# Kernel optimization log

Measured on AMD Instinct MI355X. Metric: run time of the kernel, lower is better.

Reference implementation:

```python
import jax, jax.numpy as jnp
import numpy as np

B, S, E = 4, 2048, 1024


def setup_inputs() -> dict:
    key = jax.random.key(0)
    ks = jax.random.split(key, 7)
    s = 1.0 / np.sqrt(E)  # torch Linear default init scale (uniform bound)
    inp = {
        "input": jax.random.normal(ks[0], (B, S, E), dtype=jnp.float32),
        "masked": 1,
        "W_q": jax.random.uniform(ks[1], (E, E), jnp.float32, -s, s),
        "b_q": jax.random.uniform(ks[2], (E,), jnp.float32, -s, s),
        "W_k": jax.random.uniform(ks[3], (E, E), jnp.float32, -s, s),
        "b_k": jax.random.uniform(ks[4], (E,), jnp.float32, -s, s),
        "W_v": jax.random.uniform(ks[5], (E, E), jnp.float32, -s, s),
        "b_v": jax.random.uniform(ks[6], (E,), jnp.float32, -s, s),
    }
    return inp


def reference(input, masked, W_q, b_q, W_k, b_k, W_v, b_v):
    # torch.nn.Linear: y = x @ W.T + b
    q = jnp.einsum("bse,fe->bsf", input, W_q) + b_q
    k = jnp.einsum("bse,fe->bsf", input, W_k) + b_k
    v = jnp.einsum("bse,fe->bsf", input, W_v) + b_v
    d = q.shape[-1]
    scores = jnp.einsum("bqd,bkd->bqk", q, k) / jnp.sqrt(jnp.float32(d))
    if masked:
        Sq = scores.shape[1]
        causal = jnp.tril(jnp.ones((Sq, Sq), dtype=bool))  # [S,S], broadcast over batch
        scores = jnp.where(causal, scores, -jnp.inf)
    attn = jax.nn.softmax(scores, axis=-1)
    return jnp.einsum("bqk,bkd->bqd", attn, v)
```

## Files before the change

### kernel.cpp

```cpp
#include <hip/hip_runtime.h>

typedef _Float16 f16;
typedef f16 f16x8 __attribute__((ext_vector_type(8)));
typedef f16 f16x4v __attribute__((ext_vector_type(4)));
typedef f16 f16x2v __attribute__((ext_vector_type(2)));
typedef float f32x4 __attribute__((ext_vector_type(4)));

__device__ __forceinline__ void async_ld16(const void* g, void* l) {
    __builtin_amdgcn_global_load_lds(
        (const __attribute__((address_space(1))) unsigned int*)g,
        (__attribute__((address_space(3))) unsigned int*)l, 16, 0, 0);
}

#define VMC(n) asm volatile("s_waitcnt vmcnt(" #n ")" ::: "memory")
#define BAR __builtin_amdgcn_s_barrier()


#define STG(b, op, kh, P, P1, tOff) do {                                        \
    char* d_ = (char*)smem + (b) * 65536 + (op) * 32768 + (kh) * 16384 + stgBase; \
    async_ld16((P)  + (tOff) * 64 + (kh) * 32, d_);                             \
    async_ld16((P1) + (tOff) * 64 + (kh) * 32, d_ + 8192);                      \
} while (0)
#define RD_A(b, kk) do {                                                        \
    const char* s_ = (const char*)smem + (b) * 65536 + (kk) * 16384 + aOff;     \
    _Pragma("unroll") for (int m_ = 0; m_ < 8; ++m_)                            \
        af[m_] = *(const f16x8*)(s_ + m_ * 1024);                               \
} while (0)
#define RD_B2(b, kk, n0_) do {                                                  \
    const char* s_ = (const char*)smem + (b) * 65536 + 32768 + (kk) * 16384 + bOff; \
    bf[(n0_)]     = *(const f16x8*)(s_ + ((n0_)) * 1024);                       \
    bf[(n0_) + 1] = *(const f16x8*)(s_ + ((n0_) + 1) * 1024);                   \
} while (0)
#define FENCE_MM(n0_) do {                                                      \
    __builtin_amdgcn_s_barrier();                                               \
    asm volatile("s_waitcnt lgkmcnt(0)" ::: "memory");                          \
    __builtin_amdgcn_sched_barrier(0);                                          \
    __builtin_amdgcn_s_setprio(1);                                              \
    _Pragma("unroll") for (int m_ = 0; m_ < 8; ++m_) {                          \
        acc[m_][(n0_)]     = __builtin_amdgcn_mfma_f32_16x16x32_f16(af[m_], bf[(n0_)],     acc[m_][(n0_)],     0, 0, 0); \
        acc[m_][(n0_) + 1] = __builtin_amdgcn_mfma_f32_16x16x32_f16(af[m_], bf[(n0_) + 1], acc[m_][(n0_) + 1], 0, 0, 0); \
    }                                                                           \
    __builtin_amdgcn_s_setprio(0);                                              \
} while (0)

__global__ __launch_bounds__(512, 2) void scores256(
    const f16* __restrict__ Q, const f16* __restrict__ K,
    f16* __restrict__ P, const int* __restrict__ maskedp)
{
    const int masked = *maskedp;
    const int bx = blockIdx.x, by = blockIdx.y, bz = blockIdx.z;
    if (masked && bx > by) return;
    const int mBase = by * 256, nBase = bx * 256;

    __shared__ __align__(16) f16 smem[65536];
    const int tid = threadIdx.x;
    const int wave = tid >> 6, lane = tid & 63;
    const int wrow = wave >> 2, wcol = wave & 3;
    const int quad = lane >> 4, l16 = lane & 15;
    const int rowLane = tid >> 2;
    const int cOff = ((tid & 3) ^ ((tid >> 3) & 3)) * 8;
    const int stgBase = wave * 1024;
    const int swz  = (quad ^ ((l16 >> 1) & 3)) * 16;
    const int aOff = (wrow * 128 + l16) * 64 + swz;
    const int bOff = (wcol * 64 + l16) * 64 + swz;
    f32x4 acc[8][4];
#pragma unroll
    for (int m = 0; m < 8; ++m)
#pragma unroll
        for (int n = 0; n < 4; ++n) acc[m][n] = (f32x4){0.f, 0.f, 0.f, 0.f};
    f16x8 af[8], bf[4];

    const f16* Ab  = Q + (long)bz * (2048L * 1024);
    const f16* Btb = K + (long)bz * (2048L * 1024);
    const f16* pA  = Ab  + (long)(mBase + rowLane) * 1024 + cOff;
    const f16* pA1 = pA + 128 * 1024;
    const f16* pB  = Btb + (long)(nBase + rowLane) * 1024 + cOff;
    const f16* pB1 = pB + 128 * 1024;

    STG(0, 0, 0, pA, pA1, 0); STG(0, 1, 0, pB, pB1, 0);
    STG(0, 0, 1, pA, pA1, 0); STG(0, 1, 1, pB, pB1, 0);
    STG(1, 0, 0, pA, pA1, 1); STG(1, 1, 0, pB, pB1, 1);
    VMC(4);
    BAR;

#pragma unroll 1
    for (int i = 0; i < 7; ++i) {
        RD_A(0, 0); RD_B2(0, 0, 0); STG(1, 0, 1, pA, pA1, 1);
        FENCE_MM(0); BAR;
        RD_B2(0, 0, 2);             STG(1, 1, 1, pB, pB1, 1);
        FENCE_MM(2); BAR;
        RD_A(0, 1); RD_B2(0, 1, 0); STG(0, 0, 0, pA, pA1, 2);
        FENCE_MM(0); BAR;
        RD_B2(0, 1, 2);             STG(0, 1, 0, pB, pB1, 2);
        FENCE_MM(2); VMC(4); BAR;
        RD_A(1, 0); RD_B2(1, 0, 0); STG(0, 0, 1, pA, pA1, 2);
        FENCE_MM(0); BAR;
        RD_B2(1, 0, 2);             STG(0, 1, 1, pB, pB1, 2);
        FENCE_MM(2); BAR;
        RD_A(1, 1); RD_B2(1, 1, 0); STG(1, 0, 0, pA, pA1, 3);
        FENCE_MM(0); BAR;
        RD_B2(1, 1, 2);             STG(1, 1, 0, pB, pB1, 3);
        FENCE_MM(2); VMC(4); BAR;
        pA += 128; pA1 += 128; pB += 128; pB1 += 128;
    }
    RD_A(0, 0); RD_B2(0, 0, 0); STG(1, 0, 1, pA, pA1, 1);
    FENCE_MM(0); BAR;
    RD_B2(0, 0, 2);             STG(1, 1, 1, pB, pB1, 1);
    FENCE_MM(2); BAR;
    RD_A(0, 1); RD_B2(0, 1, 0);
    FENCE_MM(0); BAR;
    RD_B2(0, 1, 2);
    FENCE_MM(2); VMC(0); BAR;
    RD_A(1, 0); RD_B2(1, 0, 0);
    FENCE_MM(0); BAR;
    RD_B2(1, 0, 2);
    FENCE_MM(2); BAR;
    RD_A(1, 1); RD_B2(1, 1, 0);
    FENCE_MM(0); BAR;
    RD_B2(1, 1, 2);
    FENCE_MM(2);

    f16* Crow = P + (long)bz * (2048L * 2048);
#pragma unroll
    for (int m = 0; m < 8; ++m)
#pragma unroll
        for (int n = 0; n < 4; ++n)
#pragma unroll
            for (int r = 0; r < 4; ++r) {
                const int row = mBase + wrow * 128 + m * 16 + quad * 4 + r;
                const int col = nBase + wcol * 64 + n * 16 + l16;
                float e = __expf(acc[m][n][r] * 0.03125f);
                if (masked && col > row) e = 0.f;
                Crow[(long)row * 2048 + col] = (f16)e;
            }
}

#undef STG
#undef RD_A
#undef RD_B2
#undef FENCE_MM

#define QSTG_A(b, kh, tOff) do {                                                \
    char* d_ = (char*)smem + (b) * 49152 + (kh) * 8192 + stgBase;               \
    async_ld16(pA + (tOff) * 64 + (kh) * 32, d_);                               \
} while (0)
#define QSTG_B(b, kh, tOff) do {                                                \
    char* d_ = (char*)smem + (b) * 49152 + 16384 + (kh) * 16384 + stgBase;      \
    async_ld16(pB  + (tOff) * 64 + (kh) * 32, d_);                              \
    async_ld16(pB1 + (tOff) * 64 + (kh) * 32, d_ + 8192);                       \
} while (0)
#define QRD(b, kk) do {                                                         \
    const char* sa_ = (const char*)smem + (b) * 49152 + (kk) * 8192 + aOff;     \
    _Pragma("unroll") for (int m_ = 0; m_ < 4; ++m_)                            \
        af[m_] = *(const f16x8*)(sa_ + m_ * 1024);                              \
    const char* sb_ = (const char*)smem + (b) * 49152 + 16384 + (kk) * 16384 + bOff; \
    _Pragma("unroll") for (int n_ = 0; n_ < 4; ++n_)                            \
        bf[n_] = *(const f16x8*)(sb_ + n_ * 1024);                              \
} while (0)
#define QFENCE do {                                                             \
    __builtin_amdgcn_s_barrier();                                               \
    asm volatile("s_waitcnt lgkmcnt(0)" ::: "memory");                          \
    __builtin_amdgcn_sched_barrier(0);                                          \
    __builtin_amdgcn_s_setprio(1);                                              \
    _Pragma("unroll") for (int m_ = 0; m_ < 4; ++m_)                            \
        _Pragma("unroll") for (int n_ = 0; n_ < 4; ++n_)                        \
            acc[m_][n_] = __builtin_amdgcn_mfma_f32_16x16x32_f16(af[m_], bf[n_], acc[m_][n_], 0, 0, 0); \
    __builtin_amdgcn_s_setprio(0);                                              \
} while (0)

__global__ __launch_bounds__(512, 2) void qkv128(
    const f16* __restrict__ A, const f16* __restrict__ Bt,
    const float* __restrict__ b_q, const float* __restrict__ b_k,
    const float* __restrict__ b_v,
    f16* __restrict__ Q16, f16* __restrict__ K16, f16* __restrict__ Vt16)
{
    int bid = blockIdx.x;
    bid = (bid & 7) * 96 + (bid >> 3);
    const int by = bid / 12, bx = bid - by * 12;
    const int mBase = by * 128, nBase = bx * 256;

    __shared__ __align__(16) f16 smem[49152];
    const int tid = threadIdx.x;
    const int wave = tid >> 6, lane = tid & 63;
    const int wrow = wave >> 2, wcol = wave & 3;
    const int quad = lane >> 4, l16 = lane & 15;
    const int rowLane = tid >> 2;
    const int cOff = ((tid & 3) ^ ((tid >> 3) & 3)) * 8;
    const int stgBase = wave * 1024;
    const int swz  = (quad ^ ((l16 >> 1) & 3)) * 16;
    const int aOff = (wrow * 64 + l16) * 64 + swz;
    const int bOff = (wcol * 64 + l16) * 64 + swz;

    const f16* pA  = A  + (long)(mBase + rowLane) * 1024 + cOff;
    const f16* pB  = Bt + (long)(nBase + rowLane) * 1024 + cOff;
    const f16* pB1 = pB + 128 * 1024;

    f32x4 acc[4][4];
#pragma unroll
    for (int m = 0; m < 4; ++m)
#pragma unroll
        for (int n = 0; n < 4; ++n) acc[m][n] = (f32x4){0.f, 0.f, 0.f, 0.f};
    f16x8 af[4], bf[4];

    QSTG_A(0, 0, 0); QSTG_B(0, 0, 0);
    QSTG_A(0, 1, 0); QSTG_B(0, 1, 0);
    QSTG_A(1, 0, 1); QSTG_B(1, 0, 1);
    VMC(3);
    BAR;

#pragma unroll 1
    for (int i = 0; i < 7; ++i) {
        QRD(0, 0); QSTG_A(1, 1, 1); QSTG_B(1, 1, 1);
        QFENCE; VMC(6); BAR;
        QRD(0, 1); QSTG_A(0, 0, 2); QSTG_B(0, 0, 2);
        QFENCE; VMC(6); BAR;
        QRD(1, 0); QSTG_A(0, 1, 2); QSTG_B(0, 1, 2);
        QFENCE; VMC(6); BAR;
        QRD(1, 1); QSTG_A(1, 0, 3); QSTG_B(1, 0, 3);
        QFENCE; VMC(6); BAR;
        pA += 128; pB += 128; pB1 += 128;
    }
    QRD(0, 0); QSTG_A(1, 1, 1); QSTG_B(1, 1, 1);
    QFENCE; VMC(6); BAR;
    QRD(0, 1);
    QFENCE; VMC(3); BAR;
    QRD(1, 0);
    QFENCE; VMC(0); BAR;
    QRD(1, 1);
    QFENCE;
    BAR;

    const int seg = nBase >> 10;
    const float* bs = (seg == 0) ? b_q : (seg == 1) ? b_k : b_v;
    const int lcb = (nBase & 1023) + wcol * 64;
    float bvv[4];
#pragma unroll
    for (int n = 0; n < 4; ++n) bvv[n] = bs[lcb + n * 16 + l16];

    if (seg < 2) {
        f16* dst = (seg == 0) ? Q16 : K16;
#pragma unroll
        for (int m = 0; m < 4; ++m)
#pragma unroll
            for (int n = 0; n < 4; ++n)
#pragma unroll
                for (int r = 0; r < 4; ++r) {
                    const int row = mBase + wrow * 64 + m * 16 + quad * 4 + r;
                    dst[(long)row * 1024 + lcb + n * 16 + l16] =
                        (f16)(acc[m][n][r] + bvv[n]);
                }
    } else {
        const int b = mBase >> 11;
        const int s0 = (mBase & 2047) + wrow * 64;
        const int e0 = (nBase & 1023) + wcol * 64;
        f16* epiW = smem + wave * (64 * 72);
#pragma unroll
        for (int m = 0; m < 4; ++m)
#pragma unroll
            for (int n = 0; n < 4; ++n) {
                f16x4v pk;
#pragma unroll
                for (int r = 0; r < 4; ++r)
                    pk[r] = (f16)(acc[m][n][r] + bvv[n]);
                *(f16x4v*)&epiW[(n * 16 + l16) * 72 + m * 16 + quad * 4] = pk;
            }
        asm volatile("s_waitcnt lgkmcnt(0)" ::: "memory");
#pragma unroll
        for (int it = 0; it < 8; ++it) {
            const int e = it * 8 + (lane >> 3);
            const f16x8 v = *(const f16x8*)&epiW[e * 72 + (lane & 7) * 8];
            *(f16x8*)(Vt16 + ((long)b * 1024 + e0 + e) * 2048 + s0 +
                      (lane & 7) * 8) = v;
        }
    }
}

#undef QSTG_A
#undef QSTG_B
#undef QRD
#undef QFENCE

#if defined(__has_builtin)
#if __has_builtin(__builtin_amdgcn_fdot2)
#define HAVE_FDOT2 1
#endif
#endif

#ifdef HAVE_FDOT2
#define PSUM do {                                                               \
    const f16x2v one_ = {(f16)1, (f16)1};                                       \
    _Pragma("unroll") for (int m_ = 0; m_ < 4; ++m_) {                          \
        const f16x2v* ph_ = (const f16x2v*)&af[m_];                             \
        _Pragma("unroll") for (int j_ = 0; j_ < 4; ++j_)                        \
            rs[m_] = __builtin_amdgcn_fdot2(ph_[j_], one_, rs[m_], false);      \
    }                                                                           \
} while (0)
#else
#define PSUM do {                                                               \
    _Pragma("unroll") for (int m_ = 0; m_ < 4; ++m_)                            \
        _Pragma("unroll") for (int j_ = 0; j_ < 8; ++j_)                        \
            rs[m_] += (float)af[m_][j_];                                        \
} while (0)
#endif

#define PSTG_A(b, kh, tOff) do {                                                \
    char* d_ = (char*)smem + (b) * 32768 + (kh) * 8192 + stgBase;               \
    async_ld16(pA  + (tOff) * 64 + (kh) * 32, d_);                              \
    async_ld16(pA1 + (tOff) * 64 + (kh) * 32, d_ + 4096);                       \
} while (0)
#define PSTG_B(b, kh, tOff) do {                                                \
    char* d_ = (char*)smem + (b) * 32768 + 16384 + (kh) * 8192 + stgBase;       \
    async_ld16(pB  + (tOff) * 64 + (kh) * 32, d_);                              \
    async_ld16(pB1 + (tOff) * 64 + (kh) * 32, d_ + 4096);                       \
} while (0)
#define PRD(b, kk) do {                                                         \
    const char* sa_ = (const char*)smem + (b) * 32768 + (kk) * 8192 + aOff;     \
    _Pragma("unroll") for (int m_ = 0; m_ < 4; ++m_)                            \
        af[m_] = *(const f16x8*)(sa_ + m_ * 1024);                              \
    const char* sb_ = (const char*)smem + (b) * 32768 + 16384 + (kk) * 8192 + bOff; \
    _Pragma("unroll") for (int n_ = 0; n_ < 4; ++n_)                            \
        bf[n_] = *(const f16x8*)(sb_ + n_ * 1024);                              \
} while (0)
#define PFENCE do {                                                             \
    __builtin_amdgcn_s_barrier();                                               \
    asm volatile("s_waitcnt lgkmcnt(0)" ::: "memory");                          \
    __builtin_amdgcn_sched_barrier(0);                                          \
    __builtin_amdgcn_s_setprio(1);                                              \
    _Pragma("unroll") for (int m_ = 0; m_ < 4; ++m_)                            \
        _Pragma("unroll") for (int n_ = 0; n_ < 4; ++n_)                        \
            acc[m_][n_] = __builtin_amdgcn_mfma_f32_16x16x32_f16(af[m_], bf[n_], acc[m_][n_], 0, 0, 0); \
    __builtin_amdgcn_s_setprio(0);                                              \
    PSUM;                                                                       \
} while (0)

__global__ __launch_bounds__(256, 2) void pv128(
    const f16* __restrict__ P, const f16* __restrict__ Vt,
    float* __restrict__ out, const int* __restrict__ maskedp)
{
    const int masked = *maskedp;
    const int bx = blockIdx.x, bz = blockIdx.z;
    const int by = (bz >= 2) ? blockIdx.y : (gridDim.y - 1 - blockIdx.y);
    const int mBase = by * 128, nBase = bx * 128;
    const int nIter = masked ? ((by >> 1) + 1) * 2 : 16;

    __shared__ __align__(16) f16 smem[32768];
    const int tid = threadIdx.x;
    const int wave = tid >> 6, lane = tid & 63;
    const int wrow = wave >> 1, wcol = wave & 1;
    const int quad = lane >> 4, l16 = lane & 15;
    const int rowLane = tid >> 2;
    const int cOff = ((tid & 3) ^ ((tid >> 3) & 3)) * 8;
    const int stgBase = wave * 1024;
    const int swz  = (quad ^ ((l16 >> 1) & 3)) * 16;
    const int aOff = (wrow * 64 + l16) * 64 + swz;
    const int bOff = (wcol * 64 + l16) * 64 + swz;

    const f16* Pb = P  + (long)bz * (2048L * 2048);
    const f16* Vb = Vt + (long)bz * (1024L * 2048);
    const f16* pA  = Pb + (long)(mBase + rowLane) * 2048 + cOff;
    const f16* pA1 = pA + 64 * 2048;
    const f16* pB  = Vb + (long)(nBase + rowLane) * 2048 + cOff;
    const f16* pB1 = pB + 64 * 2048;

    f32x4 acc[4][4];
#pragma unroll
    for (int m = 0; m < 4; ++m)
#pragma unroll
        for (int n = 0; n < 4; ++n) acc[m][n] = (f32x4){0.f, 0.f, 0.f, 0.f};
    f16x8 af[4], bf[4];
    float rs[4] = {0.f, 0.f, 0.f, 0.f};

    PSTG_A(0, 0, 0); PSTG_B(0, 0, 0);
    PSTG_A(0, 1, 0); PSTG_B(0, 1, 0);
    PSTG_A(1, 0, 1); PSTG_B(1, 0, 1);
    VMC(4);
    BAR;

#pragma unroll 1
    for (int i = 0; i < nIter - 1; ++i) {
        PRD(0, 0); PSTG_A(1, 1, 1); PSTG_B(1, 1, 1);
        PFENCE; VMC(8); BAR;
        PRD(0, 1); PSTG_A(0, 0, 2); PSTG_B(0, 0, 2);
        PFENCE; VMC(8); BAR;
        PRD(1, 0); PSTG_A(0, 1, 2); PSTG_B(0, 1, 2);
        PFENCE; VMC(8); BAR;
        PRD(1, 1); PSTG_A(1, 0, 3); PSTG_B(1, 0, 3);
        PFENCE; VMC(8); BAR;
        pA += 128; pA1 += 128; pB += 128; pB1 += 128;
    }
    PRD(0, 0); PSTG_A(1, 1, 1); PSTG_B(1, 1, 1);
    PFENCE; VMC(8); BAR;
    PRD(0, 1);
    PFENCE; VMC(4); BAR;
    PRD(1, 0);
    PFENCE; VMC(0); BAR;
    PRD(1, 1);
    PFENCE;

#pragma unroll
    for (int m = 0; m < 4; ++m) {
        rs[m] += __shfl_xor(rs[m], 16);
        rs[m] += __shfl_xor(rs[m], 32);
    }

    float* ob = out + (long)bz * (2048L * 1024);
#pragma unroll
    for (int m = 0; m < 4; ++m)
#pragma unroll
        for (int r = 0; r < 4; ++r) {
            const int row = mBase + wrow * 64 + m * 16 + quad * 4 + r;
            const float inv = 1.f / __shfl(rs[m], quad * 4 + r);
#pragma unroll
            for (int n = 0; n < 4; ++n) {
                const int col = nBase + wcol * 64 + n * 16 + l16;
                ob[(long)row * 1024 + col] = acc[m][n][r] * inv;
            }
        }
}

#undef PSTG_A
#undef PSTG_B
#undef PRD
#undef PFENCE
#undef PSUM
#undef VMC
#undef BAR

__global__ void cvt_all(const float* __restrict__ inp,
                        const float* __restrict__ W0,
                        const float* __restrict__ W1,
                        const float* __restrict__ W2,
                        f16* __restrict__ inp16, f16* __restrict__ W3)
{
    const int bxx = blockIdx.x;
    const float* src;
    f16* dst;
    int i;
    if (bxx < 8192) {
        src = inp; dst = inp16;
        i = bxx * 256 + threadIdx.x;
    } else {
        const int wb = bxx - 8192;
        const int which = wb >> 10;
        src = (which == 0) ? W0 : (which == 1) ? W1 : W2;
        dst = W3 + (long)which * 1024 * 1024;
        i = (wb & 1023) * 256 + threadIdx.x;
    }
    const float4 v = ((const float4*)src)[i];
    f16x4v o;
    o[0] = (f16)v.x; o[1] = (f16)v.y; o[2] = (f16)v.z; o[3] = (f16)v.w;
    ((f16x4v*)dst)[i] = o;
}

extern "C" void kernel_launch(void* const* d_in, const int* in_sizes, int n_in,
                              void* d_out, int out_size, void* d_ws, size_t ws_size,
                              hipStream_t stream)
{
    const float* inp = (const float*)d_in[0];
    const int* masked = (const int*)d_in[1];
    const float* Wq = (const float*)d_in[2];
    const float* bq = (const float*)d_in[3];
    const float* Wk = (const float*)d_in[4];
    const float* bk = (const float*)d_in[5];
    const float* Wv = (const float*)d_in[6];
    const float* bv = (const float*)d_in[7];
    float* out = (float*)d_out;

    const int S = 2048, E = 1024;
    const long nTok = (long)4 * S;

    char* ws = (char*)d_ws;
    f16* inp16 = (f16*)ws;   ws += nTok * E * 2;
    f16* W3    = (f16*)ws;   ws += (long)3 * E * E * 2;
    f16* Q16   = (f16*)ws;   ws += nTok * E * 2;
    f16* K16   = (f16*)ws;   ws += nTok * E * 2;
    f16* Vt16  = (f16*)ws;   ws += nTok * E * 2;
    f16* P16   = (f16*)ws;   ws += (long)4 * S * S * 2;

    cvt_all<<<dim3(8192 + 3072), dim3(256), 0, stream>>>(
        inp, Wq, Wk, Wv, inp16, W3);

    qkv128<<<dim3(768), dim3(512), 0, stream>>>(
        inp16, W3, bq, bk, bv, Q16, K16, Vt16);

    scores256<<<dim3(8, 8, 4), dim3(512), 0, stream>>>(
        Q16, K16, P16, masked);

    pv128<<<dim3(8, 16, 4), dim3(256), 0, stream>>>(
        P16, Vt16, out, masked);
}
```

Before: 238.1 us.

## Shrink score tiles to 128 for finer causal skipping and remap QKV block order

The scores kernel moves from 256x256 tiles with 512 threads to 128x128 tiles with 256 threads. With the smaller tiles the causal skip drops more of the upper triangle, and the mask check only runs on diagonal tiles. The PV kernel's iteration count now follows 128-wide granularity (by+1), so it reads fewer zero P blocks. The QKV block-to-tile mapping is changed to group rows per XCD, which may alter L2 reuse. In exchange there are more blocks, and each tile has a lower compute-to-load ratio.

```diff
diff --git a/kernel.cpp b/kernel.cpp
--- a/kernel.cpp
+++ b/kernel.cpp
@@ -16,129 +16,117 @@
 #define BAR __builtin_amdgcn_s_barrier()
 
 
-#define STG(b, op, kh, P, P1, tOff) do {                                        \
-    char* d_ = (char*)smem + (b) * 65536 + (op) * 32768 + (kh) * 16384 + stgBase; \
-    async_ld16((P)  + (tOff) * 64 + (kh) * 32, d_);                             \
-    async_ld16((P1) + (tOff) * 64 + (kh) * 32, d_ + 8192);                      \
-} while (0)
-#define RD_A(b, kk) do {                                                        \
-    const char* s_ = (const char*)smem + (b) * 65536 + (kk) * 16384 + aOff;     \
-    _Pragma("unroll") for (int m_ = 0; m_ < 8; ++m_)                            \
-        af[m_] = *(const f16x8*)(s_ + m_ * 1024);                               \
-} while (0)
-#define RD_B2(b, kk, n0_) do {                                                  \
-    const char* s_ = (const char*)smem + (b) * 65536 + 32768 + (kk) * 16384 + bOff; \
-    bf[(n0_)]     = *(const f16x8*)(s_ + ((n0_)) * 1024);                       \
-    bf[(n0_) + 1] = *(const f16x8*)(s_ + ((n0_) + 1) * 1024);                   \
-} while (0)
-#define FENCE_MM(n0_) do {                                                      \
+#define SSTG_A(b, kh, tOff) do {                                                \
+    char* d_ = (char*)smem + (b) * 32768 + (kh) * 8192 + stgBase;               \
+    async_ld16(pA  + (tOff) * 64 + (kh) * 32, d_);                              \
+    async_ld16(pA1 + (tOff) * 64 + (kh) * 32, d_ + 4096);                       \
+} while (0)
+#define SSTG_B(b, kh, tOff) do {                                                \
+    char* d_ = (char*)smem + (b) * 32768 + 16384 + (kh) * 8192 + stgBase;       \
+    async_ld16(pB  + (tOff) * 64 + (kh) * 32, d_);                              \
+    async_ld16(pB1 + (tOff) * 64 + (kh) * 32, d_ + 4096);                       \
+} while (0)
+#define SRD(b, kk) do {                                                         \
+    const char* sa_ = (const char*)smem + (b) * 32768 + (kk) * 8192 + aOff;     \
+    _Pragma("unroll") for (int m_ = 0; m_ < 4; ++m_)                            \
+        af[m_] = *(const f16x8*)(sa_ + m_ * 1024);                              \
+    const char* sb_ = (const char*)smem + (b) * 32768 + 16384 + (kk) * 8192 + bOff; \
+    _Pragma("unroll") for (int n_ = 0; n_ < 4; ++n_)                            \
+        bf[n_] = *(const f16x8*)(sb_ + n_ * 1024);                              \
+} while (0)
+#define SFENCE do {                                                             \
     __builtin_amdgcn_s_barrier();                                               \
     asm volatile("s_waitcnt lgkmcnt(0)" ::: "memory");                          \
     __builtin_amdgcn_sched_barrier(0);                                          \
     __builtin_amdgcn_s_setprio(1);                                              \
-    _Pragma("unroll") for (int m_ = 0; m_ < 8; ++m_) {                          \
-        acc[m_][(n0_)]     = __builtin_amdgcn_mfma_f32_16x16x32_f16(af[m_], bf[(n0_)],     acc[m_][(n0_)],     0, 0, 0); \
-        acc[m_][(n0_) + 1] = __builtin_amdgcn_mfma_f32_16x16x32_f16(af[m_], bf[(n0_) + 1], acc[m_][(n0_) + 1], 0, 0, 0); \
-    }                                                                           \
+    _Pragma("unroll") for (int m_ = 0; m_ < 4; ++m_)                            \
+        _Pragma("unroll") for (int n_ = 0; n_ < 4; ++n_)                        \
+            acc[m_][n_] = __builtin_amdgcn_mfma_f32_16x16x32_f16(af[m_], bf[n_], acc[m_][n_], 0, 0, 0); \
     __builtin_amdgcn_s_setprio(0);                                              \
 } while (0)
 
-__global__ __launch_bounds__(512, 2) void scores256(
+__global__ __launch_bounds__(256, 2) void scores128(
     const f16* __restrict__ Q, const f16* __restrict__ K,
     f16* __restrict__ P, const int* __restrict__ maskedp)
 {
     const int masked = *maskedp;
     const int bx = blockIdx.x, by = blockIdx.y, bz = blockIdx.z;
     if (masked && bx > by) return;
-    const int mBase = by * 256, nBase = bx * 256;
-
-    __shared__ __align__(16) f16 smem[65536];
+    const int mBase = by * 128, nBase = bx * 128;
+    const bool diag = (masked != 0) && (bx == by);
+
+    __shared__ __align__(16) f16 smem[32768];
     const int tid = threadIdx.x;
     const int wave = tid >> 6, lane = tid & 63;
-    const int wrow = wave >> 2, wcol = wave & 3;
+    const int wrow = wave >> 1, wcol = wave & 1;
     const int quad = lane >> 4, l16 = lane & 15;
     const int rowLane = tid >> 2;
     const int cOff = ((tid & 3) ^ ((tid >> 3) & 3)) * 8;
     const int stgBase = wave * 1024;
     const int swz  = (quad ^ ((l16 >> 1) & 3)) * 16;
-    const int aOff = (wrow * 128 + l16) * 64 + swz;
+    const int aOff = (wrow * 64 + l16) * 64 + swz;
     const int bOff = (wcol * 64 + l16) * 64 + swz;
-    f32x4 acc[8][4];
-#pragma unroll
-    for (int m = 0; m < 8; ++m)
+
+    const f16* Ab = Q + (long)bz * (2048L * 1024);
+    const f16* Bb = K + (long)bz * (2048L * 1024);
+    const f16* pA  = Ab + (long)(mBase + rowLane) * 1024 + cOff;
+    const f16* pA1 = pA + 64 * 1024;
+    const f16* pB  = Bb + (long)(nBase + rowLane) * 1024 + cOff;
+    const f16* pB1 = pB + 64 * 1024;
+
+    f32x4 acc[4][4];
+#pragma unroll
+    for (int m = 0; m < 4; ++m)
 #pragma unroll
         for (int n = 0; n < 4; ++n) acc[m][n] = (f32x4){0.f, 0.f, 0.f, 0.f};
-    f16x8 af[8], bf[4];
-
-    const f16* Ab  = Q + (long)bz * (2048L * 1024);
-    const f16* Btb = K + (long)bz * (2048L * 1024);
-    const f16* pA  = Ab  + (long)(mBase + rowLane) * 1024 + cOff;
-    const f16* pA1 = pA + 128 * 1024;
-    const f16* pB  = Btb + (long)(nBase + rowLane) * 1024 + cOff;
-    const f16* pB1 = pB + 128 * 1024;
-
-    STG(0, 0, 0, pA, pA1, 0); STG(0, 1, 0, pB, pB1, 0);
-    STG(0, 0, 1, pA, pA1, 0); STG(0, 1, 1, pB, pB1, 0);
-    STG(1, 0, 0, pA, pA1, 1); STG(1, 1, 0, pB, pB1, 1);
+    f16x8 af[4], bf[4];
+
+    SSTG_A(0, 0, 0); SSTG_B(0, 0, 0);
+    SSTG_A(0, 1, 0); SSTG_B(0, 1, 0);
+    SSTG_A(1, 0, 1); SSTG_B(1, 0, 1);
     VMC(4);
     BAR;
 
 #pragma unroll 1
     for (int i = 0; i < 7; ++i) {
-        RD_A(0, 0); RD_B2(0, 0, 0); STG(1, 0, 1, pA, pA1, 1);
-        FENCE_MM(0); BAR;
-        RD_B2(0, 0, 2);             STG(1, 1, 1, pB, pB1, 1);
-        FENCE_MM(2); BAR;
-        RD_A(0, 1); RD_B2(0, 1, 0); STG(0, 0, 0, pA, pA1, 2);
-        FENCE_MM(0); BAR;
-        RD_B2(0, 1, 2);             STG(0, 1, 0, pB, pB1, 2);
-        FENCE_MM(2); VMC(4); BAR;
-        RD_A(1, 0); RD_B2(1, 0, 0); STG(0, 0, 1, pA, pA1, 2);
-        FENCE_MM(0); BAR;
-        RD_B2(1, 0, 2);             STG(0, 1, 1, pB, pB1, 2);
-        FENCE_MM(2); BAR;
-        RD_A(1, 1); RD_B2(1, 1, 0); STG(1, 0, 0, pA, pA1, 3);
-        FENCE_MM(0); BAR;
-        RD_B2(1, 1, 2);             STG(1, 1, 0, pB, pB1, 3);
-        FENCE_MM(2); VMC(4); BAR;
+        SRD(0, 0); SSTG_A(1, 1, 1); SSTG_B(1, 1, 1);
+        SFENCE; VMC(8); BAR;
+        SRD(0, 1); SSTG_A(0, 0, 2); SSTG_B(0, 0, 2);
+        SFENCE; VMC(8); BAR;
+        SRD(1, 0); SSTG_A(0, 1, 2); SSTG_B(0, 1, 2);
+        SFENCE; VMC(8); BAR;
+        SRD(1, 1); SSTG_A(1, 0, 3); SSTG_B(1, 0, 3);
+        SFENCE; VMC(8); BAR;
         pA += 128; pA1 += 128; pB += 128; pB1 += 128;
     }
-    RD_A(0, 0); RD_B2(0, 0, 0); STG(1, 0, 1, pA, pA1, 1);
-    FENCE_MM(0); BAR;
-    RD_B2(0, 0, 2);             STG(1, 1, 1, pB, pB1, 1);
-    FENCE_MM(2); BAR;
-    RD_A(0, 1); RD_B2(0, 1, 0);
-    FENCE_MM(0); BAR;
-    RD_B2(0, 1, 2);
-    FENCE_MM(2); VMC(0); BAR;
-    RD_A(1, 0); RD_B2(1, 0, 0);
-    FENCE_MM(0); BAR;
-    RD_B2(1, 0, 2);
-    FENCE_MM(2); BAR;
-    RD_A(1, 1); RD_B2(1, 1, 0);
-    FENCE_MM(0); BAR;
-    RD_B2(1, 1, 2);
-    FENCE_MM(2);
+    SRD(0, 0); SSTG_A(1, 1, 1); SSTG_B(1, 1, 1);
+    SFENCE; VMC(8); BAR;
+    SRD(0, 1);
+    SFENCE; VMC(4); BAR;
+    SRD(1, 0);
+    SFENCE; VMC(0); BAR;
+    SRD(1, 1);
+    SFENCE;
 
     f16* Crow = P + (long)bz * (2048L * 2048);
 #pragma unroll
-    for (int m = 0; m < 8; ++m)
+    for (int m = 0; m < 4; ++m)
 #pragma unroll
         for (int n = 0; n < 4; ++n)
 #pragma unroll
             for (int r = 0; r < 4; ++r) {
-                const int row = mBase + wrow * 128 + m * 16 + quad * 4 + r;
+                const int row = mBase + wrow * 64 + m * 16 + quad * 4 + r;
                 const int col = nBase + wcol * 64 + n * 16 + l16;
                 float e = __expf(acc[m][n][r] * 0.03125f);
-                if (masked && col > row) e = 0.f;
+                if (diag && col > row) e = 0.f;
                 Crow[(long)row * 2048 + col] = (f16)e;
             }
 }
 
-#undef STG
-#undef RD_A
-#undef RD_B2
-#undef FENCE_MM
+#undef SSTG_A
+#undef SSTG_B
+#undef SRD
+#undef SFENCE
 
 #define QSTG_A(b, kh, tOff) do {                                                \
     char* d_ = (char*)smem + (b) * 49152 + (kh) * 8192 + stgBase;               \
@@ -174,9 +162,11 @@
     const float* __restrict__ b_v,
     f16* __restrict__ Q16, f16* __restrict__ K16, f16* __restrict__ Vt16)
 {
-    int bid = blockIdx.x;
-    bid = (bid & 7) * 96 + (bid >> 3);
-    const int by = bid / 12, bx = bid - by * 12;
+    const int orig = blockIdx.x;
+    const int xcd = orig & 7;
+    const int s = orig >> 3;
+    const int by = xcd * 8 + (s & 7);
+    const int bx = s >> 3;
     const int mBase = by * 128, nBase = bx * 256;
 
     __shared__ __align__(16) f16 smem[49152];
@@ -341,7 +331,7 @@
     const int bx = blockIdx.x, bz = blockIdx.z;
     const int by = (bz >= 2) ? blockIdx.y : (gridDim.y - 1 - blockIdx.y);
     const int mBase = by * 128, nBase = bx * 128;
-    const int nIter = masked ? ((by >> 1) + 1) * 2 : 16;
+    const int nIter = masked ? (by + 1) : 16;
 
     __shared__ __align__(16) f16 smem[32768];
     const int tid = threadIdx.x;
@@ -483,7 +473,7 @@
     qkv128<<<dim3(768), dim3(512), 0, stream>>>(
         inp16, W3, bq, bk, bv, Q16, K16, Vt16);
 
-    scores256<<<dim3(8, 8, 4), dim3(512), 0, stream>>>(
+    scores128<<<dim3(16, 16, 4), dim3(256), 0, stream>>>(
         Q16, K16, P16, masked);
 
     pv128<<<dim3(8, 16, 4), dim3(256), 0, stream>>>(
```

Result: faster. 226.5 us (-4.9%).
